# Kernel tuning notes

Hardware: AMD Instinct MI355X
Metric: run time of the kernel (lower is better)

The kernel has to match this reference:

```python
import jax, jax.numpy as jnp
import numpy as np

N_NODES = 20000
N_EDGES = 320000
N_GRAPHS = 16
NEG_SLOPE = 0.2


def gat_layer(x, src, dst, W, al, ar, b):
    # x: [N, F_in]; W: [F_in, H*D]; al/ar: [H, D]; b: [H*D]
    H, D = al.shape
    N = x.shape[0]
    f = (x @ W).reshape(N, H, D)                      # projected features [N,H,D]
    el = jnp.sum(f * al[None], axis=-1)                # [N,H]
    er = jnp.sum(f * ar[None], axis=-1)                # [N,H]
    e = jax.nn.leaky_relu(el[src] + er[dst], NEG_SLOPE)  # [E,H]
    # numerically stable segment softmax over incoming edges of each dst node
    m = jax.ops.segment_max(e, dst, num_segments=N)    # [N,H]
    m = jnp.where(jnp.isfinite(m), m, 0.0)
    ex = jnp.exp(e - m[dst])                           # [E,H]
    denom = jax.ops.segment_sum(ex, dst, num_segments=N)  # [N,H]
    msg = ex[:, :, None] * f[src]                      # [E,H,D]
    num = jax.ops.segment_sum(msg, dst, num_segments=N)   # [N,H,D]
    rst = num / jnp.where(denom > 0, denom, 1.0)[:, :, None]
    return rst + b.reshape(1, H, D)


def setup_inputs() -> dict:
    key = jax.random.key(0)
    ks = jax.random.split(key, 16)
    in_dim, hid, H = 128, 128, 3
    x = jax.random.normal(ks[0], (N_NODES, in_dim), dtype=jnp.float32)
    src = jax.random.randint(ks[1], (N_EDGES,), 0, N_NODES, dtype=jnp.int32)
    dst = jax.random.randint(ks[2], (N_EDGES,), 0, N_NODES, dtype=jnp.int32)
    graph_ids = jnp.sort(jax.random.randint(ks[3], (N_NODES,), 0, N_GRAPHS, dtype=jnp.int32))
    s = lambda d: 1.0 / np.sqrt(d)
    W1 = jax.random.normal(ks[4], (in_dim, H * hid), jnp.float32) * s(in_dim)
    al1 = jax.random.normal(ks[5], (H, hid), jnp.float32) * s(hid)
    ar1 = jax.random.normal(ks[6], (H, hid), jnp.float32) * s(hid)
    b1 = jnp.zeros((H * hid,), jnp.float32)
    W2 = jax.random.normal(ks[7], (H * hid, hid), jnp.float32) * s(H * hid)
    al2 = jax.random.normal(ks[8], (1, hid), jnp.float32) * s(hid)
    ar2 = jax.random.normal(ks[9], (1, hid), jnp.float32) * s(hid)
    b2 = jnp.zeros((hid,), jnp.float32)
    linW = jax.random.normal(ks[10], (hid, hid), jnp.float32) * s(hid)
    linb = jnp.zeros((hid,), jnp.float32)
    return dict(x=x, src=src, dst=dst, graph_ids=graph_ids, W1=W1, al1=al1,
                ar1=ar1, b1=b1, W2=W2, al2=al2, ar2=ar2, b2=b2, linW=linW, linb=linb)


def reference(x, src, dst, graph_ids, W1, al1, ar1, b1, W2, al2, ar2, b2, linW, linb):
    h = gat_layer(x, src, dst, W1, al1, ar1, b1)       # [N,3,hid]
    h = jax.nn.elu(h.reshape(h.shape[0], -1))          # [N,3*hid]
    h = gat_layer(h, src, dst, W2, al2, ar2, b2)       # [N,1,hid]
    h = h.squeeze(1)                                   # [N,hid]
    # dgl.mean_nodes over batched graph
    sums = jax.ops.segment_sum(h, graph_ids, num_segments=N_GRAPHS)      # [G,hid]
    cnts = jax.ops.segment_sum(jnp.ones_like(graph_ids, jnp.float32), graph_ids, num_segments=N_GRAPHS)
    hg = sums / jnp.maximum(cnts, 1.0)[:, None]
    return jax.nn.relu(hg @ linW + linb)
```

## Files before the change

### kernel.cpp

```cpp
#include <hip/hip_runtime.h>
#include <hip/hip_bf16.h>

#define NN 20000
#define NE 320000
#define NG 16
#define PSPLIT 32


__global__ void hist_kernel(const int* __restrict__ dst, int* __restrict__ indeg, int E) {
  int e = blockIdx.x * 256 + threadIdx.x;
  if (e < E) atomicAdd(&indeg[dst[e]], 1);
}

__global__ void exscan_kernel(const int* __restrict__ in, int* __restrict__ outp, int n) {
  __shared__ int wsum[16];
  __shared__ int wexcl[16];
  __shared__ int tot_s;
  __shared__ int carry_s;
  int t = threadIdx.x;
  int lane = t & 63, wv = t >> 6;
  if (t == 0) carry_s = 0;
  __syncthreads();
  for (int base = 0; base < n; base += 1024) {
    int i = base + t;
    int v = (i < n) ? in[i] : 0;
    int x = v;
#pragma unroll
    for (int off = 1; off < 64; off <<= 1) {
      int y = __shfl_up(x, off);
      if (lane >= off) x += y;
    }
    if (lane == 63) wsum[wv] = x;
    __syncthreads();
    int carry = carry_s;
    if (t < 16) {
      int s = wsum[t];
      int xs = s;
#pragma unroll
      for (int off = 1; off < 16; off <<= 1) {
        int y = __shfl_up(xs, off);
        if (t >= off) xs += y;
      }
      wexcl[t] = xs - s;
      if (t == 15) tot_s = xs;
    }
    __syncthreads();
    if (i < n) outp[i] = carry + wexcl[wv] + (x - v);
    if (t == 0) carry_s = carry + tot_s;
  }
  if (t == 0) outp[n] = carry_s;
}

__global__ void scatter_kernel(const int* __restrict__ src, const int* __restrict__ dst,
                               const int* __restrict__ rowptr, int* __restrict__ cursor,
                               int* __restrict__ csr_src, int E) {
  int e = blockIdx.x * 256 + threadIdx.x;
  if (e < E) {
    int d = dst[e];
    int p = atomicAdd(&cursor[d], 1);
    csr_src[rowptr[d] + p] = src[e];
  }
}


__global__ void prep_wlr_kernel(const float* __restrict__ W1, const float* __restrict__ al1,
                                const float* __restrict__ ar1, float* __restrict__ wlr) {
  int t = blockIdx.x * 256 + threadIdx.x;
  if (t >= 768) return;
  int k = t & 127;
  int j = t >> 7;
  int h = j % 3;
  const float* av = (j < 3 ? al1 : ar1) + h * 128;
  const float* wrow = W1 + (size_t)k * 384 + h * 128;
  float s = 0.f;
#pragma unroll 4
  for (int d = 0; d < 128; d++) s += wrow[d] * av[d];
  wlr[j * 128 + k] = s;
}

__global__ void elr_kernel(const float* __restrict__ x, const float* __restrict__ wlr,
                           float* __restrict__ el, float* __restrict__ er, int N) {
  __shared__ float wl_s[768];
  int t = threadIdx.x;
  for (int i = t; i < 768; i += 256) wl_s[i] = wlr[i];
  __syncthreads();
  int w = (blockIdx.x * 256 + t) >> 6;
  int lane = t & 63;
  if (w >= N) return;
  float v0 = x[(size_t)w * 128 + lane], v1 = x[(size_t)w * 128 + 64 + lane];
  float s[6];
#pragma unroll
  for (int j = 0; j < 6; j++) s[j] = v0 * wl_s[j * 128 + lane] + v1 * wl_s[j * 128 + 64 + lane];
#pragma unroll
  for (int off = 32; off; off >>= 1)
#pragma unroll
    for (int j = 0; j < 6; j++) s[j] += __shfl_down(s[j], off);
  if (lane == 0) {
    el[w * 3 + 0] = s[0]; el[w * 3 + 1] = s[1]; el[w * 3 + 2] = s[2];
    er[w * 3 + 0] = s[3]; er[w * 3 + 1] = s[4]; er[w * 3 + 2] = s[5];
  }
}


__global__ void aggregate_x_kernel(const float* __restrict__ x, const float* __restrict__ el,
                                   const float* __restrict__ er, const int* __restrict__ rowptr,
                                   const int* __restrict__ csr_src, float* __restrict__ aggx) {
  int n = blockIdx.x;
  int t = threadIdx.x;
  __shared__ float wbuf[3][128];
  __shared__ int sbuf[128];
  __shared__ float red[6];
  __shared__ float4 accbuf[3][4][32];
  int rs = rowptr[n];
  int deg = rowptr[n + 1] - rs;
  float er0 = er[n * 3 + 0], er1 = er[n * 3 + 1], er2 = er[n * 3 + 2];
  float p0 = 0.f, p1 = 0.f, p2 = 0.f;
  int g = t >> 5, dq = t & 31;
  const float* xd = x + dq * 4;
  float4 a0 = make_float4(0, 0, 0, 0), a1 = a0, a2 = a0;
  for (int base = 0; base < deg; base += 128) {
    int cnt = min(128, deg - base);
    if (t < cnt) {
      int s = csr_src[rs + base + t];
      sbuf[t] = s;
      float e0 = el[s * 3 + 0] + er0, e1 = el[s * 3 + 1] + er1, e2 = el[s * 3 + 2] + er2;
      e0 = e0 > 0.f ? e0 : 0.2f * e0;
      e1 = e1 > 0.f ? e1 : 0.2f * e1;
      e2 = e2 > 0.f ? e2 : 0.2f * e2;
      float w0 = __expf(e0), w1 = __expf(e1), w2 = __expf(e2);
      wbuf[0][t] = w0; wbuf[1][t] = w1; wbuf[2][t] = w2;
      p0 += w0; p1 += w1; p2 += w2;
    }
    __syncthreads();
    int j = g;
    for (; j + 4 < cnt; j += 8) {
      int s0 = sbuf[j], s1 = sbuf[j + 4];
      float4 v0 = *(const float4*)(xd + (size_t)s0 * 128);
      float4 v1 = *(const float4*)(xd + (size_t)s1 * 128);
      float w00 = wbuf[0][j], w01 = wbuf[1][j], w02 = wbuf[2][j];
      float w10 = wbuf[0][j + 4], w11 = wbuf[1][j + 4], w12 = wbuf[2][j + 4];
      a0.x += w00 * v0.x + w10 * v1.x; a0.y += w00 * v0.y + w10 * v1.y;
      a0.z += w00 * v0.z + w10 * v1.z; a0.w += w00 * v0.w + w10 * v1.w;
      a1.x += w01 * v0.x + w11 * v1.x; a1.y += w01 * v0.y + w11 * v1.y;
      a1.z += w01 * v0.z + w11 * v1.z; a1.w += w01 * v0.w + w11 * v1.w;
      a2.x += w02 * v0.x + w12 * v1.x; a2.y += w02 * v0.y + w12 * v1.y;
      a2.z += w02 * v0.z + w12 * v1.z; a2.w += w02 * v0.w + w12 * v1.w;
    }
    for (; j < cnt; j += 4) {
      int s = sbuf[j];
      float4 v = *(const float4*)(xd + (size_t)s * 128);
      float w0 = wbuf[0][j], w1 = wbuf[1][j], w2 = wbuf[2][j];
      a0.x += w0 * v.x; a0.y += w0 * v.y; a0.z += w0 * v.z; a0.w += w0 * v.w;
      a1.x += w1 * v.x; a1.y += w1 * v.y; a1.z += w1 * v.z; a1.w += w1 * v.w;
      a2.x += w2 * v.x; a2.y += w2 * v.y; a2.z += w2 * v.z; a2.w += w2 * v.w;
    }
    __syncthreads();
  }
  for (int off = 32; off; off >>= 1) {
    p0 += __shfl_down(p0, off);
    p1 += __shfl_down(p1, off);
    p2 += __shfl_down(p2, off);
  }
  int wv = t >> 6, ln = t & 63;
  if (ln == 0) { red[wv * 3 + 0] = p0; red[wv * 3 + 1] = p1; red[wv * 3 + 2] = p2; }
  accbuf[0][g][dq] = a0;
  accbuf[1][g][dq] = a1;
  accbuf[2][g][dq] = a2;
  __syncthreads();
  if (t < 96) {
    int h = t >> 5, d = t & 31;
    float4 s0 = accbuf[h][0][d], s1 = accbuf[h][1][d], s2 = accbuf[h][2][d], s3 = accbuf[h][3][d];
    float dn = red[h] + red[3 + h];
    float inv = dn > 0.f ? 1.f / dn : 0.f;
    float4 r;
    r.x = (s0.x + s1.x + s2.x + s3.x) * inv;
    r.y = (s0.y + s1.y + s2.y + s3.y) * inv;
    r.z = (s0.z + s1.z + s2.z + s3.z) * inv;
    r.w = (s0.w + s1.w + s2.w + s3.w) * inv;
    *(float4*)&aggx[(size_t)n * 384 + h * 128 + d * 4] = r;
  }
}


template <int K, bool BIAS_ELU>
__launch_bounds__(256)
__global__ void gemm64e_kernel(const float* __restrict__ A, int lda, int sA,
                               const float* __restrict__ B, int ldb, int sB,
                               float* __restrict__ C, int ldc, int sC,
                               const float* __restrict__ bias, int sBias, int M) {
  __shared__ float As[64 * 36];
  __shared__ float Bs[32 * 128];
  int hy = blockIdx.y;
  A += (size_t)hy * sA; B += (size_t)hy * sB; C += (size_t)hy * sC;
  if (BIAS_ELU) bias += (size_t)hy * sBias;
  int t = threadIdx.x;
  int m0 = blockIdx.x * 64;
  int tm = t >> 4, tn = t & 15;
  float acc[4][8];
#pragma unroll
  for (int i = 0; i < 4; i++)
#pragma unroll
    for (int j = 0; j < 8; j++) acc[i][j] = 0.f;

  for (int k0 = 0; k0 < K; k0 += 32) {
#pragma unroll
    for (int i = 0; i < 2; i++) {
      int idx = t + i * 256;
      int r = idx >> 3, kq = (idx & 7) * 4;
      int gm = m0 + r;
      float4 v = make_float4(0.f, 0.f, 0.f, 0.f);
      if (gm < M) v = *(const float4*)&A[(size_t)gm * lda + k0 + kq];
      *(float4*)&As[r * 36 + kq] = v;
    }
#pragma unroll
    for (int i = 0; i < 4; i++) {
      int idx = t + i * 256;
      int kk = idx >> 5, nq = (idx & 31) * 4;
      float4 v = *(const float4*)&B[(size_t)(k0 + kk) * ldb + nq];
      *(float4*)&Bs[kk * 128 + nq] = v;
    }
    __syncthreads();
#pragma unroll 8
    for (int k = 0; k < 32; k++) {
      float af[4];
#pragma unroll
      for (int i = 0; i < 4; i++) af[i] = As[(tm * 4 + i) * 36 + k];
      float4 b0 = *(const float4*)&Bs[k * 128 + tn * 4];
      float4 b1 = *(const float4*)&Bs[k * 128 + 64 + tn * 4];
      float bf[8] = {b0.x, b0.y, b0.z, b0.w, b1.x, b1.y, b1.z, b1.w};
#pragma unroll
      for (int i = 0; i < 4; i++)
#pragma unroll
        for (int j = 0; j < 8; j++) acc[i][j] += af[i] * bf[j];
    }
    __syncthreads();
  }
  float bv[8];
  if (BIAS_ELU) {
#pragma unroll
    for (int j = 0; j < 4; j++) { bv[j] = bias[tn * 4 + j]; bv[4 + j] = bias[64 + tn * 4 + j]; }
  }
#pragma unroll
  for (int i = 0; i < 4; i++) {
    int gm = m0 + tm * 4 + i;
    if (gm < M) {
      float r[8];
#pragma unroll
      for (int j = 0; j < 8; j++) {
        float v = acc[i][j];
        if (BIAS_ELU) {
          v += bv[j];
          v = v > 0.f ? v : expm1f(v);
        }
        r[j] = v;
      }
      *(float4*)&C[(size_t)gm * ldc + tn * 4] = make_float4(r[0], r[1], r[2], r[3]);
      *(float4*)&C[(size_t)gm * ldc + 64 + tn * 4] = make_float4(r[4], r[5], r[6], r[7]);
    }
  }
}


__global__ void att_coef_kernel(const float* __restrict__ f, const float* __restrict__ al,
                                const float* __restrict__ ar, float* __restrict__ el,
                                float* __restrict__ er, int NH) {
  int w = (blockIdx.x * 256 + threadIdx.x) >> 6;
  int lane = threadIdx.x & 63;
  if (w >= NH) return;
  const float* fr = f + (size_t)w * 128;
  float v0 = fr[lane], v1 = fr[64 + lane];
  float a0 = al[lane], a1 = al[64 + lane];
  float r0 = ar[lane], r1 = ar[64 + lane];
  float se = v0 * a0 + v1 * a1;
  float sr = v0 * r0 + v1 * r1;
  for (int off = 32; off; off >>= 1) {
    se += __shfl_down(se, off);
    sr += __shfl_down(sr, off);
  }
  if (lane == 0) { el[w] = se; er[w] = sr; }
}


__global__ void aggregate1_kernel(const float* __restrict__ f, const float* __restrict__ el,
                                  const float* __restrict__ er, const float* __restrict__ bias,
                                  const int* __restrict__ rowptr, const int* __restrict__ csr_src,
                                  float* __restrict__ out) {
  int n = blockIdx.x;
  int t = threadIdx.x;
  __shared__ float wbuf[128];
  __shared__ int sbuf[128];
  __shared__ float red[2];
  __shared__ float4 accbuf[4][32];
  int rs = rowptr[n];
  int deg = rowptr[n + 1] - rs;
  float ern = er[n];
  float psum = 0.f;
  int g = t >> 5;
  int d = (t & 31) * 4;
  const float* fd = f + d;
  float4 acc = make_float4(0.f, 0.f, 0.f, 0.f);
  for (int base = 0; base < deg; base += 128) {
    int cnt = min(128, deg - base);
    if (t < cnt) {
      int s = csr_src[rs + base + t];
      sbuf[t] = s;
      float e = el[s] + ern;
      e = e > 0.f ? e : 0.2f * e;
      float w = __expf(e);
      wbuf[t] = w;
      psum += w;
    }
    __syncthreads();
    int j = g;
    for (; j + 4 < cnt; j += 8) {
      int s0 = sbuf[j], s1 = sbuf[j + 4];
      float4 v0 = *(const float4*)(fd + (size_t)s0 * 128);
      float4 v1 = *(const float4*)(fd + (size_t)s1 * 128);
      float w0 = wbuf[j], w1 = wbuf[j + 4];
      acc.x += w0 * v0.x + w1 * v1.x;
      acc.y += w0 * v0.y + w1 * v1.y;
      acc.z += w0 * v0.z + w1 * v1.z;
      acc.w += w0 * v0.w + w1 * v1.w;
    }
    for (; j < cnt; j += 4) {
      int s = sbuf[j];
      float4 v = *(const float4*)(fd + (size_t)s * 128);
      float w = wbuf[j];
      acc.x += w * v.x; acc.y += w * v.y; acc.z += w * v.z; acc.w += w * v.w;
    }
    __syncthreads();
  }
  for (int off = 32; off; off >>= 1) psum += __shfl_down(psum, off);
  int wv = t >> 6, ln = t & 63;
  if (ln == 0) red[wv] = psum;
  accbuf[g][t & 31] = acc;
  __syncthreads();
  if (t < 32) {
    float4 a0 = accbuf[0][t], a1 = accbuf[1][t], a2 = accbuf[2][t], a3 = accbuf[3][t];
    float dn = red[0] + red[1];
    float inv = dn > 0.f ? 1.f / dn : 0.f;
    const float* bp = bias + t * 4;
    float4 r;
    r.x = (a0.x + a1.x + a2.x + a3.x) * inv + bp[0];
    r.y = (a0.y + a1.y + a2.y + a3.y) * inv + bp[1];
    r.z = (a0.z + a1.z + a2.z + a3.z) * inv + bp[2];
    r.w = (a0.w + a1.w + a2.w + a3.w) * inv + bp[3];
    *(float4*)&out[(size_t)n * 128 + t * 4] = r;
  }
}


__global__ void pool_partial_kernel(const float* __restrict__ h2, const int* __restrict__ gid,
                                    float* __restrict__ sums, int N) {
  int g = blockIdx.x / PSPLIT;
  int sp = blockIdx.x % PSPLIT;
  int tid = threadIdx.x;
  int lo0 = 0, hi0 = N;
  while (lo0 < hi0) { int m = (lo0 + hi0) >> 1; if (gid[m] < g) lo0 = m + 1; else hi0 = m; }
  int lo1 = lo0, hi1 = N;
  while (lo1 < hi1) { int m = (lo1 + hi1) >> 1; if (gid[m] < g + 1) lo1 = m + 1; else hi1 = m; }
  float a0 = 0.f, a1 = 0.f, a2 = 0.f, a3 = 0.f;
  int n = lo0 + sp;
  for (; n + 3 * PSPLIT < lo1; n += 4 * PSPLIT) {
    a0 += h2[(size_t)n * 128 + tid];
    a1 += h2[(size_t)(n + PSPLIT) * 128 + tid];
    a2 += h2[(size_t)(n + 2 * PSPLIT) * 128 + tid];
    a3 += h2[(size_t)(n + 3 * PSPLIT) * 128 + tid];
  }
  for (; n < lo1; n += PSPLIT) a0 += h2[(size_t)n * 128 + tid];
  float acc = (a0 + a1) + (a2 + a3);
  atomicAdd(&sums[g * 128 + tid], acc);
}

__global__ void pool_final_kernel(const float* __restrict__ sums, const int* __restrict__ gid,
                                  const float* __restrict__ linW, const float* __restrict__ linb,
                                  float* __restrict__ out, int N) {
  int g = blockIdx.x;
  int tid = threadIdx.x;
  int lo0 = 0, hi0 = N;
  while (lo0 < hi0) { int m = (lo0 + hi0) >> 1; if (gid[m] < g) lo0 = m + 1; else hi0 = m; }
  int lo1 = lo0, hi1 = N;
  while (lo1 < hi1) { int m = (lo1 + hi1) >> 1; if (gid[m] < g + 1) lo1 = m + 1; else hi1 = m; }
  int cnt = lo1 - lo0;
  float hg = sums[g * 128 + tid] / (float)(cnt > 0 ? cnt : 1);
  __shared__ float hgs[128];
  hgs[tid] = hg;
  __syncthreads();
  float o = linb[tid];
#pragma unroll 4
  for (int dd = 0; dd < 128; dd++) o += hgs[dd] * linW[dd * 128 + tid];
  out[g * 128 + tid] = fmaxf(o, 0.f);
}


extern "C" void kernel_launch(void* const* d_in, const int* in_sizes, int n_in,
                              void* d_out, int out_size, void* d_ws, size_t ws_size,
                              hipStream_t stream) {
  const float* x    = (const float*)d_in[0];
  const int*   src  = (const int*)d_in[1];
  const int*   dst  = (const int*)d_in[2];
  const int*   gid  = (const int*)d_in[3];
  const float* W1   = (const float*)d_in[4];
  const float* al1  = (const float*)d_in[5];
  const float* ar1  = (const float*)d_in[6];
  const float* b1   = (const float*)d_in[7];
  const float* W2   = (const float*)d_in[8];
  const float* al2  = (const float*)d_in[9];
  const float* ar2  = (const float*)d_in[10];
  const float* b2   = (const float*)d_in[11];
  const float* linW = (const float*)d_in[12];
  const float* linb = (const float*)d_in[13];
  float* out = (float*)d_out;

  char* ws = (char*)d_ws;
  size_t off = 0;
  auto alloc = [&](size_t bytes) -> void* {
    void* p = ws + off;
    off += (bytes + 255) & ~(size_t)255;
    return p;
  };
  float* aggx    = (float*)alloc((size_t)NN * 384 * 4);
  float* h1      = (float*)alloc((size_t)NN * 384 * 4);
  float* f2      = (float*)alloc((size_t)NN * 128 * 4);
  float* h2      = (float*)alloc((size_t)NN * 128 * 4);
  float* el1     = (float*)alloc((size_t)NN * 3 * 4);
  float* er1     = (float*)alloc((size_t)NN * 3 * 4);
  float* el2     = (float*)alloc((size_t)NN * 4);
  float* er2     = (float*)alloc((size_t)NN * 4);
  float* wlr     = (float*)alloc((size_t)768 * 4);
  int*   rowptr  = (int*)alloc((size_t)(NN + 1) * 4);
  int*   csr_src = (int*)alloc((size_t)NE * 4);
  int*   indeg   = (int*)alloc((size_t)NN * 4);
  int*   cursor  = (int*)alloc((size_t)NN * 4);
  float* gsums   = (float*)alloc((size_t)NG * 128 * 4);
  (void)ws_size;
  size_t zbytes = (char*)(gsums + NG * 128) - (char*)indeg;
  hipMemsetAsync(indeg, 0, zbytes, stream);

  hist_kernel<<<(NE + 255) / 256, 256, 0, stream>>>(dst, indeg, NE);
  exscan_kernel<<<1, 1024, 0, stream>>>(indeg, rowptr, NN);
  scatter_kernel<<<(NE + 255) / 256, 256, 0, stream>>>(src, dst, rowptr, cursor, csr_src, NE);

  prep_wlr_kernel<<<3, 256, 0, stream>>>(W1, al1, ar1, wlr);
  elr_kernel<<<(NN + 3) / 4, 256, 0, stream>>>(x, wlr, el1, er1, NN);
  aggregate_x_kernel<<<NN, 128, 0, stream>>>(x, el1, er1, rowptr, csr_src, aggx);
  gemm64e_kernel<128, true><<<dim3(313, 3), 256, 0, stream>>>(
      aggx, 384, 128, W1, 384, 128, h1, 384, 128, b1, 128, NN);

  gemm64e_kernel<384, false><<<dim3(313, 1), 256, 0, stream>>>(
      h1, 384, 0, W2, 128, 0, f2, 128, 0, nullptr, 0, NN);
  att_coef_kernel<<<(NN + 3) / 4, 256, 0, stream>>>(f2, al2, ar2, el2, er2, NN);
  aggregate1_kernel<<<NN, 128, 0, stream>>>(f2, el2, er2, b2, rowptr, csr_src, h2);

  pool_partial_kernel<<<NG * PSPLIT, 128, 0, stream>>>(h2, gid, gsums, NN);
  pool_final_kernel<<<NG, 128, 0, stream>>>(gsums, gid, linW, linb, out, NN);
}
```

Before: 316.0 us.

## Parallelize degree scan across blocks and retile GEMMs to 32x64 tiles

```diff
diff --git a/kernel.cpp b/kernel.cpp
--- a/kernel.cpp
+++ b/kernel.cpp
@@ -5,6 +5,7 @@
 #define NE 320000
 #define NG 16
 #define PSPLIT 32
+#define NSCANB 79
 
 
 __global__ void hist_kernel(const int* __restrict__ dst, int* __restrict__ indeg, int E) {
@@ -12,43 +13,50 @@
   if (e < E) atomicAdd(&indeg[dst[e]], 1);
 }
 
-__global__ void exscan_kernel(const int* __restrict__ in, int* __restrict__ outp, int n) {
-  __shared__ int wsum[16];
-  __shared__ int wexcl[16];
-  __shared__ int tot_s;
-  __shared__ int carry_s;
+__global__ void scan1_kernel(const int* __restrict__ in, int* __restrict__ outp,
+                             int* __restrict__ bsum, int n) {
+  int b = blockIdx.x, t = threadIdx.x;
+  int i = b * 256 + t;
+  int lane = t & 63, wv = t >> 6;
+  __shared__ int ws[4];
+  int v = (i < n) ? in[i] : 0;
+  int x = v;
+#pragma unroll
+  for (int off = 1; off < 64; off <<= 1) {
+    int y = __shfl_up(x, off);
+    if (lane >= off) x += y;
+  }
+  if (lane == 63) ws[wv] = x;
+  __syncthreads();
+  int add = 0;
+  for (int w2 = 0; w2 < wv; w2++) add += ws[w2];
+  x += add;
+  if (i < n) outp[i] = x - v;
+  if (t == 255) bsum[b] = x;
+}
+
+__global__ void scan2_kernel(const int* __restrict__ bsum, int* __restrict__ boff,
+                             int* __restrict__ rp_end, int nb) {
   int t = threadIdx.x;
   int lane = t & 63, wv = t >> 6;
-  if (t == 0) carry_s = 0;
-  __syncthreads();
-  for (int base = 0; base < n; base += 1024) {
-    int i = base + t;
-    int v = (i < n) ? in[i] : 0;
-    int x = v;
-#pragma unroll
-    for (int off = 1; off < 64; off <<= 1) {
-      int y = __shfl_up(x, off);
-      if (lane >= off) x += y;
-    }
-    if (lane == 63) wsum[wv] = x;
-    __syncthreads();
-    int carry = carry_s;
-    if (t < 16) {
-      int s = wsum[t];
-      int xs = s;
-#pragma unroll
-      for (int off = 1; off < 16; off <<= 1) {
-        int y = __shfl_up(xs, off);
-        if (t >= off) xs += y;
-      }
-      wexcl[t] = xs - s;
-      if (t == 15) tot_s = xs;
-    }
-    __syncthreads();
-    if (i < n) outp[i] = carry + wexcl[wv] + (x - v);
-    if (t == 0) carry_s = carry + tot_s;
-  }
-  if (t == 0) outp[n] = carry_s;
+  __shared__ int ws[2];
+  int v = (t < nb) ? bsum[t] : 0;
+  int x = v;
+#pragma unroll
+  for (int off = 1; off < 64; off <<= 1) {
+    int y = __shfl_up(x, off);
+    if (lane >= off) x += y;
+  }
+  if (lane == 63) ws[wv] = x;
+  __syncthreads();
+  if (wv == 1) x += ws[0];
+  if (t < nb) boff[t] = x - v;
+  if (t == 127) *rp_end = x;
+}
+
+__global__ void scan3_kernel(int* __restrict__ outp, const int* __restrict__ boff, int n) {
+  int i = blockIdx.x * 256 + threadIdx.x;
+  if (i < n) outp[i] += boff[blockIdx.x];
 }
 
 __global__ void scatter_kernel(const int* __restrict__ src, const int* __restrict__ dst,
@@ -182,81 +190,75 @@
 }
 
 
-template <int K, bool BIAS_ELU>
-__launch_bounds__(256)
-__global__ void gemm64e_kernel(const float* __restrict__ A, int lda, int sA,
-                               const float* __restrict__ B, int ldb, int sB,
-                               float* __restrict__ C, int ldc, int sC,
-                               const float* __restrict__ bias, int sBias, int M) {
-  __shared__ float As[64 * 36];
-  __shared__ float Bs[32 * 128];
-  int hy = blockIdx.y;
-  A += (size_t)hy * sA; B += (size_t)hy * sB; C += (size_t)hy * sC;
-  if (BIAS_ELU) bias += (size_t)hy * sBias;
+template <int K, bool HEADS, bool BIAS_ELU>
+__launch_bounds__(128)
+__global__ void gemm3264_kernel(const float* __restrict__ A, int lda,
+                                const float* __restrict__ B, int ldb,
+                                float* __restrict__ C, int ldc,
+                                const float* __restrict__ bias) {
+  __shared__ float As[32 * 40];
+  __shared__ float Bs[32 * 64];
   int t = threadIdx.x;
-  int m0 = blockIdx.x * 64;
+  int m0 = blockIdx.x * 32;
+  int col0 = blockIdx.y * 64;
+  if (HEADS) A += (size_t)(col0 >> 7) * 128;
   int tm = t >> 4, tn = t & 15;
-  float acc[4][8];
+  float acc[4][4];
 #pragma unroll
   for (int i = 0; i < 4; i++)
 #pragma unroll
-    for (int j = 0; j < 8; j++) acc[i][j] = 0.f;
+    for (int j = 0; j < 4; j++) acc[i][j] = 0.f;
 
   for (int k0 = 0; k0 < K; k0 += 32) {
 #pragma unroll
     for (int i = 0; i < 2; i++) {
-      int idx = t + i * 256;
+      int idx = t + i * 128;
       int r = idx >> 3, kq = (idx & 7) * 4;
-      int gm = m0 + r;
-      float4 v = make_float4(0.f, 0.f, 0.f, 0.f);
-      if (gm < M) v = *(const float4*)&A[(size_t)gm * lda + k0 + kq];
-      *(float4*)&As[r * 36 + kq] = v;
+      float4 v = *(const float4*)&A[(size_t)(m0 + r) * lda + k0 + kq];
+      As[(kq + 0) * 40 + r] = v.x;
+      As[(kq + 1) * 40 + r] = v.y;
+      As[(kq + 2) * 40 + r] = v.z;
+      As[(kq + 3) * 40 + r] = v.w;
     }
 #pragma unroll
     for (int i = 0; i < 4; i++) {
-      int idx = t + i * 256;
-      int kk = idx >> 5, nq = (idx & 31) * 4;
-      float4 v = *(const float4*)&B[(size_t)(k0 + kk) * ldb + nq];
-      *(float4*)&Bs[kk * 128 + nq] = v;
-    }
-    __syncthreads();
-#pragma unroll 8
+      int idx = t + i * 128;
+      int kk = idx >> 4, nq = (idx & 15) * 4;
+      *(float4*)&Bs[kk * 64 + nq] = *(const float4*)&B[(size_t)(k0 + kk) * ldb + col0 + nq];
+    }
+    __syncthreads();
+#pragma unroll
     for (int k = 0; k < 32; k++) {
-      float af[4];
-#pragma unroll
-      for (int i = 0; i < 4; i++) af[i] = As[(tm * 4 + i) * 36 + k];
-      float4 b0 = *(const float4*)&Bs[k * 128 + tn * 4];
-      float4 b1 = *(const float4*)&Bs[k * 128 + 64 + tn * 4];
-      float bf[8] = {b0.x, b0.y, b0.z, b0.w, b1.x, b1.y, b1.z, b1.w};
+      float4 a = *(const float4*)&As[k * 40 + tm * 4];
+      float4 b = *(const float4*)&Bs[k * 64 + tn * 4];
+      float af[4] = {a.x, a.y, a.z, a.w};
+      float bf[4] = {b.x, b.y, b.z, b.w};
 #pragma unroll
       for (int i = 0; i < 4; i++)
 #pragma unroll
-        for (int j = 0; j < 8; j++) acc[i][j] += af[i] * bf[j];
-    }
-    __syncthreads();
-  }
-  float bv[8];
+        for (int j = 0; j < 4; j++) acc[i][j] += af[i] * bf[j];
+    }
+    __syncthreads();
+  }
+  float bv[4];
   if (BIAS_ELU) {
 #pragma unroll
-    for (int j = 0; j < 4; j++) { bv[j] = bias[tn * 4 + j]; bv[4 + j] = bias[64 + tn * 4 + j]; }
+    for (int j = 0; j < 4; j++) bv[j] = bias[col0 + tn * 4 + j];
   }
 #pragma unroll
   for (int i = 0; i < 4; i++) {
     int gm = m0 + tm * 4 + i;
-    if (gm < M) {
-      float r[8];
-#pragma unroll
-      for (int j = 0; j < 8; j++) {
-        float v = acc[i][j];
-        if (BIAS_ELU) {
-          v += bv[j];
-          v = v > 0.f ? v : expm1f(v);
-        }
-        r[j] = v;
+    float r[4];
+#pragma unroll
+    for (int j = 0; j < 4; j++) {
+      float v = acc[i][j];
+      if (BIAS_ELU) {
+        v += bv[j];
+        v = v > 0.f ? v : expm1f(v);
       }
-      *(float4*)&C[(size_t)gm * ldc + tn * 4] = make_float4(r[0], r[1], r[2], r[3]);
-      *(float4*)&C[(size_t)gm * ldc + 64 + tn * 4] = make_float4(r[4], r[5], r[6], r[7]);
-    }
+      r[j] = v;
+    }
+    *(float4*)&C[(size_t)gm * ldc + col0 + tn * 4] = make_float4(r[0], r[1], r[2], r[3]);
   }
 }
 
@@ -430,6 +432,8 @@
   float* wlr     = (float*)alloc((size_t)768 * 4);
   int*   rowptr  = (int*)alloc((size_t)(NN + 1) * 4);
   int*   csr_src = (int*)alloc((size_t)NE * 4);
+  int*   bsum    = (int*)alloc((size_t)NSCANB * 4);
+  int*   boff    = (int*)alloc((size_t)NSCANB * 4);
   int*   indeg   = (int*)alloc((size_t)NN * 4);
   int*   cursor  = (int*)alloc((size_t)NN * 4);
   float* gsums   = (float*)alloc((size_t)NG * 128 * 4);
@@ -438,17 +442,19 @@
   hipMemsetAsync(indeg, 0, zbytes, stream);
 
   hist_kernel<<<(NE + 255) / 256, 256, 0, stream>>>(dst, indeg, NE);
-  exscan_kernel<<<1, 1024, 0, stream>>>(indeg, rowptr, NN);
+  scan1_kernel<<<NSCANB, 256, 0, stream>>>(indeg, rowptr, bsum, NN);
+  scan2_kernel<<<1, 128, 0, stream>>>(bsum, boff, rowptr + NN, NSCANB);
+  scan3_kernel<<<NSCANB, 256, 0, stream>>>(rowptr, boff, NN);
   scatter_kernel<<<(NE + 255) / 256, 256, 0, stream>>>(src, dst, rowptr, cursor, csr_src, NE);
 
   prep_wlr_kernel<<<3, 256, 0, stream>>>(W1, al1, ar1, wlr);
   elr_kernel<<<(NN + 3) / 4, 256, 0, stream>>>(x, wlr, el1, er1, NN);
   aggregate_x_kernel<<<NN, 128, 0, stream>>>(x, el1, er1, rowptr, csr_src, aggx);
-  gemm64e_kernel<128, true><<<dim3(313, 3), 256, 0, stream>>>(
-      aggx, 384, 128, W1, 384, 128, h1, 384, 128, b1, 128, NN);
-
-  gemm64e_kernel<384, false><<<dim3(313, 1), 256, 0, stream>>>(
-      h1, 384, 0, W2, 128, 0, f2, 128, 0, nullptr, 0, NN);
+  gemm3264_kernel<128, true, true><<<dim3(625, 6), 128, 0, stream>>>(
+      aggx, 384, W1, 384, h1, 384, b1);
+
+  gemm3264_kernel<384, false, false><<<dim3(625, 2), 128, 0, stream>>>(
+      h1, 384, W2, 128, f2, 128, nullptr);
   att_coef_kernel<<<(NN + 3) / 4, 256, 0, stream>>>(f2, al2, ar2, el2, er2, NN);
   aggregate1_kernel<<<NN, 128, 0, stream>>>(f2, el2, er2, b2, rowptr, csr_src, h2);
 
```

Result: faster. 290.5 us (-8.1%).
